# Performance work log

Measured on AMD Instinct MI355X. Metric: run time of the kernel, lower is better.

## Reference

```python
import jax, jax.numpy as jnp
import numpy as np

HIDDEN = 32          # hardcoded in nn.Linear(latent_dim, 32)
THRESHOLD = 1.5      # hardcoded adjacency threshold


def setup_inputs() -> dict:
    key = jax.random.key(0)
    ks = jax.random.split(key, 12)
    N, LATENT, MSG = 8192, 128, 64

    def lin(kw, kb, fan_in, fan_out):
        bound = 1.0 / np.sqrt(fan_in)
        W = jax.random.uniform(kw, (fan_in, fan_out), jnp.float32, -bound, bound)
        b = jax.random.uniform(kb, (fan_out,), jnp.float32, -bound, bound)
        return W, b

    enc_W, enc_b = lin(ks[0], ks[1], LATENT, HIDDEN)
    msg_W, msg_b = lin(ks[2], ks[3], HIDDEN, MSG)
    upd_W, upd_b = lin(ks[4], ks[5], HIDDEN + MSG, HIDDEN)
    out_W, out_b = lin(ks[6], ks[7], HIDDEN, MSG)

    z = jax.random.normal(ks[8], (N, LATENT), jnp.float32)
    agent_dists = jax.random.normal(ks[9], (N, N), jnp.float32)
    tau = jnp.float32(1.0)
    return {
        "z": z, "tau": tau, "agent_dists": agent_dists,
        "enc_W": enc_W, "enc_b": enc_b,
        "msg_W": msg_W, "msg_b": msg_b,
        "upd_W": upd_W, "upd_b": upd_b,
        "out_W": out_W, "out_b": out_b,
    }


def reference(z, tau, agent_dists, enc_W, enc_b, msg_W, msg_b, upd_W, upd_b, out_W, out_b):
    N = agent_dists.shape[0]
    h = jax.nn.relu(z @ enc_W + enc_b)                       # [N, 32]
    # vectorized adjacency: off-diagonal entries with dist < threshold
    idx = jnp.arange(N)
    off_diag = idx[:, None] != idx[None, :]
    adj = jnp.where(off_diag & (agent_dists < THRESHOLD), 1.0, 0.0).astype(z.dtype)  # [N, N]
    messages = h @ msg_W + msg_b                             # [N, MSG]
    aggregated = adj @ messages                              # [N, MSG]
    h2 = jax.nn.relu(jnp.concatenate([h, aggregated], axis=-1) @ upd_W + upd_b)  # [N, 32]
    logits = h2 @ out_W + out_b                              # [N, MSG]
    # gumbel_softmax (soft): softmax((logits + gumbel) / tau)
    gkey = jax.random.key(42)
    u = jax.random.uniform(gkey, logits.shape, logits.dtype, 1e-10, 1.0)
    gumbel = -jnp.log(-jnp.log(u))
    return jax.nn.softmax((logits + gumbel) / tau, axis=-1)
```

## Files before the change

### kernel.cpp

```cpp
#include <hip/hip_runtime.h>
#include <hip/hip_bf16.h>
#include <math.h>

#define N_AGENTS 8192
#define LATENT   128
#define HIDDEN   32
#define MSG      64
#define CONCAT   96
#define THRESH   1.5f
#define NPART    16
#define ROWSTRIDE 260

typedef float f32x4  __attribute__((ext_vector_type(4)));
typedef short bf16x8 __attribute__((ext_vector_type(8)));

__device__ __forceinline__ unsigned rotl32(unsigned x, unsigned r) {
  return (x << r) | (x >> (32u - r));
}
__device__ __forceinline__ void tf_round(unsigned &x0, unsigned &x1, unsigned r) {
  x0 += x1; x1 = rotl32(x1, r); x1 ^= x0;
}
__device__ __forceinline__ uint2 threefry_0_42(unsigned x0, unsigned x1) {
  const unsigned k0 = 0u, k1 = 42u, k2 = 0x1BD11BDAu ^ 0u ^ 42u;
  x0 += k0; x1 += k1;
  tf_round(x0,x1,13); tf_round(x0,x1,15); tf_round(x0,x1,26); tf_round(x0,x1, 6);
  x0 += k1; x1 += k2 + 1u;
  tf_round(x0,x1,17); tf_round(x0,x1,29); tf_round(x0,x1,16); tf_round(x0,x1,24);
  x0 += k2; x1 += k0 + 2u;
  tf_round(x0,x1,13); tf_round(x0,x1,15); tf_round(x0,x1,26); tf_round(x0,x1, 6);
  x0 += k0; x1 += k1 + 3u;
  tf_round(x0,x1,17); tf_round(x0,x1,29); tf_round(x0,x1,16); tf_round(x0,x1,24);
  x0 += k1; x1 += k2 + 4u;
  tf_round(x0,x1,13); tf_round(x0,x1,15); tf_round(x0,x1,26); tf_round(x0,x1, 6);
  x0 += k2; x1 += k0 + 5u;
  return make_uint2(x0, x1);
}

__device__ __forceinline__ float gumbel_at(unsigned idx) {
  const unsigned H = (N_AGENTS * MSG) / 2;
  unsigned bits;
  if (idx < H) {
    uint2 o = threefry_0_42(idx, idx + H);
    bits = o.x;
  } else {
    uint2 o = threefry_0_42(idx - H, idx);
    bits = o.y;
  }
  float f = __uint_as_float((bits >> 9) | 0x3f800000u) - 1.0f;
  float u = fmaxf(1e-10f, f + 1e-10f);
  return -logf(-logf(u));
}

__device__ __forceinline__ unsigned short f2bf(float x) {
  unsigned u = __float_as_uint(x);
  u += 0x7FFFu + ((u >> 16) & 1u);
  return (unsigned short)(u >> 16);
}

__device__ __forceinline__ void stage16(const float* g, float* l) {
  __builtin_amdgcn_global_load_lds(
      (const __attribute__((address_space(1))) void*)g,
      (__attribute__((address_space(3))) void*)l, 16, 0, 0);
}

__global__ __launch_bounds__(256) void k_encode(
    const float* __restrict__ z, const float* __restrict__ encW, const float* __restrict__ encB,
    const float* __restrict__ msgW, const float* __restrict__ msgB,
    float* __restrict__ h_out, unsigned* __restrict__ msgR_u32,
    unsigned short* __restrict__ msgT)
{
  __shared__ float z_s[8][LATENT];
  __shared__ float encW_s[LATENT*HIDDEN];
  __shared__ float msgW_s[HIDDEN*MSG];
  __shared__ float h_s[8][HIDDEN];
  __shared__ float m_s[8][MSG];
  const int t  = threadIdx.x;
  const int r0 = blockIdx.x * 8;

  #pragma unroll
  for (int it = 0; it < 16; ++it) encW_s[t + 256*it] = encW[t + 256*it];
  #pragma unroll
  for (int it = 0; it < 8; ++it)  msgW_s[t + 256*it] = msgW[t + 256*it];
  #pragma unroll
  for (int it = 0; it < 4; ++it) {
    int q = t + 256*it;
    z_s[q >> 7][q & 127] = z[(size_t)r0*LATENT + q];
  }
  __syncthreads();

  {
    int r = t >> 5, c = t & 31;
    float acc = encB[c];
    #pragma unroll
    for (int k = 0; k < LATENT; ++k) acc = fmaf(z_s[r][k], encW_s[k*HIDDEN + c], acc);
    float hv = fmaxf(acc, 0.0f);
    h_s[r][c] = hv;
    h_out[(size_t)(r0 + r)*HIDDEN + c] = hv;
  }
  __syncthreads();

  #pragma unroll
  for (int it = 0; it < 2; ++it) {
    int r = (t >> 6) + 4*it, c = t & 63;
    float acc = msgB[c];
    #pragma unroll
    for (int k = 0; k < HIDDEN; ++k) acc = fmaf(h_s[r][k], msgW_s[k*MSG + c], acc);
    m_s[r][c] = acc;
  }
  __syncthreads();

  {
    int r = t >> 5, c0 = (t & 31) * 2;
    unsigned lo = f2bf(m_s[r][c0]), hi = f2bf(m_s[r][c0 + 1]);
    msgR_u32[(size_t)(r0 + r)*32 + (t & 31)] = lo | (hi << 16);
  }
  {
    int c = t & 63, rr = (t >> 6) * 2;
    unsigned lo = f2bf(m_s[rr][c]), hi = f2bf(m_s[rr + 1][c]);
    *(unsigned*)(msgT + (size_t)c*N_AGENTS + r0 + rr) = lo | (hi << 16);
  }
}

__device__ __forceinline__ bf16x8 adj_frag(f32x4 lo, f32x4 hi) {
  union { bf16x8 v; unsigned u[4]; } r;
  r.u[0] = (lo.x < THRESH ? 0x3F80u : 0u) | (lo.y < THRESH ? 0x3F800000u : 0u);
  r.u[1] = (lo.z < THRESH ? 0x3F80u : 0u) | (lo.w < THRESH ? 0x3F800000u : 0u);
  r.u[2] = (hi.x < THRESH ? 0x3F80u : 0u) | (hi.y < THRESH ? 0x3F800000u : 0u);
  r.u[3] = (hi.z < THRESH ? 0x3F80u : 0u) | (hi.w < THRESH ? 0x3F800000u : 0u);
  return r.v;
}

__global__ __launch_bounds__(256, 4) void k_agg(
    const float* __restrict__ dists, const unsigned short* __restrict__ msgT,
    float* __restrict__ P)
{
  __shared__ __align__(16) float ldsA[32 * ROWSTRIDE];
  const int lane = threadIdx.x & 63;
  const int wv   = threadIdx.x >> 6;
  const int rowTile  = blockIdx.x & 255;
  const int sliceGrp = blockIdx.x >> 8;
  const int row0 = rowTile * 32;
  const int kblk = sliceGrp * 2048;
  const int m = lane & 15, q = lane >> 4;

  f32x4 acc[2][4];
  #pragma unroll
  for (int g = 0; g < 2; ++g)
    #pragma unroll
    for (int nt = 0; nt < 4; ++nt) acc[g][nt] = (f32x4)0.0f;

  const unsigned short* bbase = msgT + (size_t)m * N_AGENTS;

  for (int chunk = 0; chunk < 8; ++chunk) {
    const int kb = kblk + chunk * 256;
    #pragma unroll
    for (int rr = 0; rr < 8; ++rr) {
      const int r = wv * 8 + rr;
      stage16(dists + (size_t)(row0 + r) * N_AGENTS + kb + lane * 4,
              &ldsA[r * ROWSTRIDE]);
    }
    __syncthreads();

    #pragma unroll
    for (int ks = 0; ks < 2; ++ks) {
      const int kf = wv * 64 + ks * 32 + q * 8;
      f32x4 a00 = *(const f32x4*)&ldsA[m * ROWSTRIDE + kf];
      f32x4 a01 = *(const f32x4*)&ldsA[m * ROWSTRIDE + kf + 4];
      f32x4 a10 = *(const f32x4*)&ldsA[(m + 16) * ROWSTRIDE + kf];
      f32x4 a11 = *(const f32x4*)&ldsA[(m + 16) * ROWSTRIDE + kf + 4];
      bf16x8 af0 = adj_frag(a00, a01);
      bf16x8 af1 = adj_frag(a10, a11);
      const size_t kg = (size_t)kb + kf;
      bf16x8 b0 = *(const bf16x8*)(bbase + (size_t)0  * N_AGENTS + kg);
      bf16x8 b1 = *(const bf16x8*)(bbase + (size_t)16 * N_AGENTS + kg);
      bf16x8 b2 = *(const bf16x8*)(bbase + (size_t)32 * N_AGENTS + kg);
      bf16x8 b3 = *(const bf16x8*)(bbase + (size_t)48 * N_AGENTS + kg);
      acc[0][0] = __builtin_amdgcn_mfma_f32_16x16x32_bf16(af0, b0, acc[0][0], 0, 0, 0);
      acc[0][1] = __builtin_amdgcn_mfma_f32_16x16x32_bf16(af0, b1, acc[0][1], 0, 0, 0);
      acc[0][2] = __builtin_amdgcn_mfma_f32_16x16x32_bf16(af0, b2, acc[0][2], 0, 0, 0);
      acc[0][3] = __builtin_amdgcn_mfma_f32_16x16x32_bf16(af0, b3, acc[0][3], 0, 0, 0);
      acc[1][0] = __builtin_amdgcn_mfma_f32_16x16x32_bf16(af1, b0, acc[1][0], 0, 0, 0);
      acc[1][1] = __builtin_amdgcn_mfma_f32_16x16x32_bf16(af1, b1, acc[1][1], 0, 0, 0);
      acc[1][2] = __builtin_amdgcn_mfma_f32_16x16x32_bf16(af1, b2, acc[1][2], 0, 0, 0);
      acc[1][3] = __builtin_amdgcn_mfma_f32_16x16x32_bf16(af1, b3, acc[1][3], 0, 0, 0);
    }
    __syncthreads();
  }

  float* dst = P + (size_t)(sliceGrp * 4 + wv) * N_AGENTS * MSG;
  #pragma unroll
  for (int g = 0; g < 2; ++g)
    #pragma unroll
    for (int nt = 0; nt < 4; ++nt)
      #pragma unroll
      for (int r = 0; r < 4; ++r)
        dst[(size_t)(row0 + g*16 + q*4 + r) * MSG + nt*16 + m] = acc[g][nt][r];
}

__global__ __launch_bounds__(256) void k_out(
    const float* __restrict__ P, const float* __restrict__ dists,
    const unsigned short* __restrict__ msgR,
    const float* __restrict__ h_in,
    const float* __restrict__ updW, const float* __restrict__ updB,
    const float* __restrict__ outW, const float* __restrict__ outB,
    const float* __restrict__ tau, float* __restrict__ out)
{
  __shared__ float x_s[4][CONCAT];
  __shared__ float h2_s[4][HIDDEN];
  const int w    = threadIdx.x >> 6;
  const int lane = threadIdx.x & 63;
  const int i    = blockIdx.x * 4 + w;

  float agg = 0.0f;
  #pragma unroll
  for (int g = 0; g < NPART; ++g)
    agg += P[((size_t)g * N_AGENTS + i) * MSG + lane];

  float dii = dists[(size_t)i * (N_AGENTS + 1)];
  if (dii < THRESH) {
    unsigned short us = msgR[(size_t)i * MSG + lane];
    agg -= __uint_as_float(((unsigned)us) << 16);
  }

  x_s[w][HIDDEN + lane] = agg;
  if (lane < HIDDEN) x_s[w][lane] = h_in[(size_t)i * HIDDEN + lane];
  __syncthreads();

  if (lane < HIDDEN) {
    float acc = updB[lane];
    #pragma unroll
    for (int k = 0; k < CONCAT; ++k) acc = fmaf(x_s[w][k], updW[k*HIDDEN + lane], acc);
    h2_s[w][lane] = fmaxf(acc, 0.0f);
  }
  __syncthreads();

  float lg = outB[lane];
  #pragma unroll
  for (int c = 0; c < HIDDEN; ++c) lg = fmaf(h2_s[w][c], outW[c*MSG + lane], lg);

  float tv = (lg + gumbel_at((unsigned)i*64u + (unsigned)lane)) / tau[0];

  float mx = tv;
  #pragma unroll
  for (int off = 32; off > 0; off >>= 1) mx = fmaxf(mx, __shfl_xor(mx, off, 64));
  float ex = expf(tv - mx);
  float sm = ex;
  #pragma unroll
  for (int off = 32; off > 0; off >>= 1) sm += __shfl_xor(sm, off, 64);
  out[(size_t)i * MSG + lane] = ex / sm;
}

extern "C" void kernel_launch(void* const* d_in, const int* in_sizes, int n_in,
                              void* d_out, int out_size, void* d_ws, size_t ws_size,
                              hipStream_t stream) {
  const float* z     = (const float*)d_in[0];
  const float* tau   = (const float*)d_in[1];
  const float* dists = (const float*)d_in[2];
  const float* encW  = (const float*)d_in[3];
  const float* encB  = (const float*)d_in[4];
  const float* msgW  = (const float*)d_in[5];
  const float* msgB  = (const float*)d_in[6];
  const float* updW  = (const float*)d_in[7];
  const float* updB  = (const float*)d_in[8];
  const float* outW  = (const float*)d_in[9];
  const float* outB  = (const float*)d_in[10];
  (void)in_sizes; (void)n_in; (void)out_size; (void)ws_size;

  char* ws = (char*)d_ws;
  float*          P_ws  = (float*)(ws);
  float*          h_ws  = (float*)(ws + (32u<<20));
  unsigned short* msgR  = (unsigned short*)(ws + (33u<<20));
  unsigned short* msgT  = (unsigned short*)(ws + (34u<<20));
  float* out = (float*)d_out;

  hipLaunchKernelGGL(k_encode, dim3(N_AGENTS/8), dim3(256), 0, stream,
                     z, encW, encB, msgW, msgB, h_ws, (unsigned*)msgR, msgT);
  hipLaunchKernelGGL(k_agg, dim3(256 * 4), dim3(256), 0, stream,
                     dists, msgT, P_ws);
  hipLaunchKernelGGL(k_out, dim3(N_AGENTS/4), dim3(256), 0, stream,
                     P_ws, dists, msgR, h_ws, updW, updB, outW, outB, tau, out);
}
```

Measured before the change: 418.5 us.

## Fuse aggregation and output MLP into one kernel with double-buffered dist staging

Merges the adjacency-aggregation kernel and the output/update/softmax kernel. Each block now owns 16 full rows across the whole K dimension, so the 16-way partial-sum buffer written to global memory and re-read by a second kernel goes away, along with one launch. It also double-buffers the dists tiles in LDS so the next chunk loads while the current one is computed. The trade-off is fewer, longer-running blocks (512 instead of 1024) and a larger LDS footprint per block, which may lower occupancy and memory parallelism on the dominant 256MB dists stream.

```diff
diff --git a/kernel.cpp b/kernel.cpp
--- a/kernel.cpp
+++ b/kernel.cpp
@@ -1,5 +1,4 @@
 #include <hip/hip_runtime.h>
-#include <hip/hip_bf16.h>
 #include <math.h>
 
 #define N_AGENTS 8192
@@ -8,8 +7,11 @@
 #define MSG      64
 #define CONCAT   96
 #define THRESH   1.5f
-#define NPART    16
-#define ROWSTRIDE 260
+
+#define ROWS     16
+#define CHUNK    512
+#define NCHUNK   (N_AGENTS / CHUNK)
+#define RSTR     516
 
 typedef float f32x4  __attribute__((ext_vector_type(4)));
 typedef short bf16x8 __attribute__((ext_vector_type(8)));
@@ -130,124 +132,129 @@
   return r.v;
 }
 
-__global__ __launch_bounds__(256, 4) void k_agg(
+__global__ __launch_bounds__(256, 2) void k_fused(
     const float* __restrict__ dists, const unsigned short* __restrict__ msgT,
-    float* __restrict__ P)
+    const unsigned short* __restrict__ msgR, const float* __restrict__ h_in,
+    const float* __restrict__ updW, const float* __restrict__ updB,
+    const float* __restrict__ outW, const float* __restrict__ outB,
+    const float* __restrict__ tau, float* __restrict__ out)
 {
-  __shared__ __align__(16) float ldsA[32 * ROWSTRIDE];
+  __shared__ __align__(16) float S[2 * ROWS * RSTR];
   const int lane = threadIdx.x & 63;
   const int wv   = threadIdx.x >> 6;
-  const int rowTile  = blockIdx.x & 255;
-  const int sliceGrp = blockIdx.x >> 8;
-  const int row0 = rowTile * 32;
-  const int kblk = sliceGrp * 2048;
   const int m = lane & 15, q = lane >> 4;
-
-  f32x4 acc[2][4];
-  #pragma unroll
-  for (int g = 0; g < 2; ++g)
-    #pragma unroll
-    for (int nt = 0; nt < 4; ++nt) acc[g][nt] = (f32x4)0.0f;
+  const int row0 = blockIdx.x * ROWS;
+  const int wvK  = wv * 128;
+
+  f32x4 acc[4];
+  #pragma unroll
+  for (int nt = 0; nt < 4; ++nt) acc[nt] = (f32x4)0.0f;
 
   const unsigned short* bbase = msgT + (size_t)m * N_AGENTS;
 
-  for (int chunk = 0; chunk < 8; ++chunk) {
-    const int kb = kblk + chunk * 256;
-    #pragma unroll
-    for (int rr = 0; rr < 8; ++rr) {
-      const int r = wv * 8 + rr;
-      stage16(dists + (size_t)(row0 + r) * N_AGENTS + kb + lane * 4,
-              &ldsA[r * ROWSTRIDE]);
-    }
-    __syncthreads();
-
-    #pragma unroll
-    for (int ks = 0; ks < 2; ++ks) {
-      const int kf = wv * 64 + ks * 32 + q * 8;
-      f32x4 a00 = *(const f32x4*)&ldsA[m * ROWSTRIDE + kf];
-      f32x4 a01 = *(const f32x4*)&ldsA[m * ROWSTRIDE + kf + 4];
-      f32x4 a10 = *(const f32x4*)&ldsA[(m + 16) * ROWSTRIDE + kf];
-      f32x4 a11 = *(const f32x4*)&ldsA[(m + 16) * ROWSTRIDE + kf + 4];
-      bf16x8 af0 = adj_frag(a00, a01);
-      bf16x8 af1 = adj_frag(a10, a11);
-      const size_t kg = (size_t)kb + kf;
+  #pragma unroll
+  for (int rr = 0; rr < 4; ++rr) {
+    const int r = wv * 4 + rr;
+    const float* gsrc = dists + (size_t)(row0 + r) * N_AGENTS;
+    stage16(gsrc + lane * 4,       &S[r * RSTR]);
+    stage16(gsrc + 256 + lane * 4, &S[r * RSTR + 256]);
+  }
+  __syncthreads();
+
+  for (int c = 0; c < NCHUNK; ++c) {
+    float* buf = &S[(c & 1) * ROWS * RSTR];
+    if (c + 1 < NCHUNK) {
+      float* nbuf = &S[((c + 1) & 1) * ROWS * RSTR];
+      const int cb = (c + 1) * CHUNK;
+      #pragma unroll
+      for (int rr = 0; rr < 4; ++rr) {
+        const int r = wv * 4 + rr;
+        const float* gsrc = dists + (size_t)(row0 + r) * N_AGENTS + cb;
+        stage16(gsrc + lane * 4,       &nbuf[r * RSTR]);
+        stage16(gsrc + 256 + lane * 4, &nbuf[r * RSTR + 256]);
+      }
+    }
+    const int cb0 = c * CHUNK;
+    #pragma unroll
+    for (int ks = 0; ks < 4; ++ks) {
+      const int kf = wvK + ks * 32 + q * 8;
+      f32x4 a0 = *(const f32x4*)&buf[m * RSTR + kf];
+      f32x4 a1 = *(const f32x4*)&buf[m * RSTR + kf + 4];
+      bf16x8 af = adj_frag(a0, a1);
+      const size_t kg = (size_t)cb0 + kf;
       bf16x8 b0 = *(const bf16x8*)(bbase + (size_t)0  * N_AGENTS + kg);
       bf16x8 b1 = *(const bf16x8*)(bbase + (size_t)16 * N_AGENTS + kg);
       bf16x8 b2 = *(const bf16x8*)(bbase + (size_t)32 * N_AGENTS + kg);
       bf16x8 b3 = *(const bf16x8*)(bbase + (size_t)48 * N_AGENTS + kg);
-      acc[0][0] = __builtin_amdgcn_mfma_f32_16x16x32_bf16(af0, b0, acc[0][0], 0, 0, 0);
-      acc[0][1] = __builtin_amdgcn_mfma_f32_16x16x32_bf16(af0, b1, acc[0][1], 0, 0, 0);
-      acc[0][2] = __builtin_amdgcn_mfma_f32_16x16x32_bf16(af0, b2, acc[0][2], 0, 0, 0);
-      acc[0][3] = __builtin_amdgcn_mfma_f32_16x16x32_bf16(af0, b3, acc[0][3], 0, 0, 0);
-      acc[1][0] = __builtin_amdgcn_mfma_f32_16x16x32_bf16(af1, b0, acc[1][0], 0, 0, 0);
-      acc[1][1] = __builtin_amdgcn_mfma_f32_16x16x32_bf16(af1, b1, acc[1][1], 0, 0, 0);
-      acc[1][2] = __builtin_amdgcn_mfma_f32_16x16x32_bf16(af1, b2, acc[1][2], 0, 0, 0);
-      acc[1][3] = __builtin_amdgcn_mfma_f32_16x16x32_bf16(af1, b3, acc[1][3], 0, 0, 0);
+      acc[0] = __builtin_amdgcn_mfma_f32_16x16x32_bf16(af, b0, acc[0], 0, 0, 0);
+      acc[1] = __builtin_amdgcn_mfma_f32_16x16x32_bf16(af, b1, acc[1], 0, 0, 0);
+      acc[2] = __builtin_amdgcn_mfma_f32_16x16x32_bf16(af, b2, acc[2], 0, 0, 0);
+      acc[3] = __builtin_amdgcn_mfma_f32_16x16x32_bf16(af, b3, acc[3], 0, 0, 0);
     }
     __syncthreads();
   }
 
-  float* dst = P + (size_t)(sliceGrp * 4 + wv) * N_AGENTS * MSG;
-  #pragma unroll
-  for (int g = 0; g < 2; ++g)
-    #pragma unroll
-    for (int nt = 0; nt < 4; ++nt)
+  float* part = S;
+  #pragma unroll
+  for (int nt = 0; nt < 4; ++nt)
+    #pragma unroll
+    for (int r = 0; r < 4; ++r)
+      part[wv * 1024 + (q * 4 + r) * 64 + nt * 16 + m] = acc[nt][r];
+  __syncthreads();
+
+  float* x_s  = &S[8192];
+  float* h2_s = &S[8192 + 16 * CONCAT];
+  const float tauv = tau[0];
+
+  #pragma unroll
+  for (int rr = 0; rr < 4; ++rr) {
+    const int r16 = wv * 4 + rr;
+    const int i = row0 + r16;
+    float agg = part[0 * 1024 + r16 * 64 + lane]
+              + part[1 * 1024 + r16 * 64 + lane]
+              + part[2 * 1024 + r16 * 64 + lane]
+              + part[3 * 1024 + r16 * 64 + lane];
+    float dii = dists[(size_t)i * (N_AGENTS + 1)];
+    if (dii < THRESH) {
+      unsigned short us = msgR[(size_t)i * MSG + lane];
+      agg -= __uint_as_float(((unsigned)us) << 16);
+    }
+    x_s[r16 * CONCAT + HIDDEN + lane] = agg;
+    if (lane < HIDDEN) x_s[r16 * CONCAT + lane] = h_in[(size_t)i * HIDDEN + lane];
+  }
+
+  #pragma unroll
+  for (int rr = 0; rr < 4; ++rr) {
+    const int r16 = wv * 4 + rr;
+    if (lane < HIDDEN) {
+      float a2 = updB[lane];
       #pragma unroll
-      for (int r = 0; r < 4; ++r)
-        dst[(size_t)(row0 + g*16 + q*4 + r) * MSG + nt*16 + m] = acc[g][nt][r];
-}
-
-__global__ __launch_bounds__(256) void k_out(
-    const float* __restrict__ P, const float* __restrict__ dists,
-    const unsigned short* __restrict__ msgR,
-    const float* __restrict__ h_in,
-    const float* __restrict__ updW, const float* __restrict__ updB,
-    const float* __restrict__ outW, const float* __restrict__ outB,
-    const float* __restrict__ tau, float* __restrict__ out)
-{
-  __shared__ float x_s[4][CONCAT];
-  __shared__ float h2_s[4][HIDDEN];
-  const int w    = threadIdx.x >> 6;
-  const int lane = threadIdx.x & 63;
-  const int i    = blockIdx.x * 4 + w;
-
-  float agg = 0.0f;
-  #pragma unroll
-  for (int g = 0; g < NPART; ++g)
-    agg += P[((size_t)g * N_AGENTS + i) * MSG + lane];
-
-  float dii = dists[(size_t)i * (N_AGENTS + 1)];
-  if (dii < THRESH) {
-    unsigned short us = msgR[(size_t)i * MSG + lane];
-    agg -= __uint_as_float(((unsigned)us) << 16);
-  }
-
-  x_s[w][HIDDEN + lane] = agg;
-  if (lane < HIDDEN) x_s[w][lane] = h_in[(size_t)i * HIDDEN + lane];
-  __syncthreads();
-
-  if (lane < HIDDEN) {
-    float acc = updB[lane];
-    #pragma unroll
-    for (int k = 0; k < CONCAT; ++k) acc = fmaf(x_s[w][k], updW[k*HIDDEN + lane], acc);
-    h2_s[w][lane] = fmaxf(acc, 0.0f);
-  }
-  __syncthreads();
-
-  float lg = outB[lane];
-  #pragma unroll
-  for (int c = 0; c < HIDDEN; ++c) lg = fmaf(h2_s[w][c], outW[c*MSG + lane], lg);
-
-  float tv = (lg + gumbel_at((unsigned)i*64u + (unsigned)lane)) / tau[0];
-
-  float mx = tv;
-  #pragma unroll
-  for (int off = 32; off > 0; off >>= 1) mx = fmaxf(mx, __shfl_xor(mx, off, 64));
-  float ex = expf(tv - mx);
-  float sm = ex;
-  #pragma unroll
-  for (int off = 32; off > 0; off >>= 1) sm += __shfl_xor(sm, off, 64);
-  out[(size_t)i * MSG + lane] = ex / sm;
+      for (int k = 0; k < CONCAT; ++k)
+        a2 = fmaf(x_s[r16 * CONCAT + k], updW[k * HIDDEN + lane], a2);
+      h2_s[r16 * HIDDEN + lane] = fmaxf(a2, 0.0f);
+    }
+  }
+
+  #pragma unroll
+  for (int rr = 0; rr < 4; ++rr) {
+    const int r16 = wv * 4 + rr;
+    const int i = row0 + r16;
+    float lg = outB[lane];
+    #pragma unroll
+    for (int c = 0; c < HIDDEN; ++c)
+      lg = fmaf(h2_s[r16 * HIDDEN + c], outW[c * MSG + lane], lg);
+
+    float tv = (lg + gumbel_at((unsigned)i * 64u + (unsigned)lane)) / tauv;
+
+    float mx = tv;
+    #pragma unroll
+    for (int off = 32; off > 0; off >>= 1) mx = fmaxf(mx, __shfl_xor(mx, off, 64));
+    float ex = expf(tv - mx);
+    float sm = ex;
+    #pragma unroll
+    for (int off = 32; off > 0; off >>= 1) sm += __shfl_xor(sm, off, 64);
+    out[(size_t)i * MSG + lane] = ex / sm;
+  }
 }
 
 extern "C" void kernel_launch(void* const* d_in, const int* in_sizes, int n_in,
@@ -267,16 +274,13 @@
   (void)in_sizes; (void)n_in; (void)out_size; (void)ws_size;
 
   char* ws = (char*)d_ws;
-  float*          P_ws  = (float*)(ws);
-  float*          h_ws  = (float*)(ws + (32u<<20));
-  unsigned short* msgR  = (unsigned short*)(ws + (33u<<20));
-  unsigned short* msgT  = (unsigned short*)(ws + (34u<<20));
+  float*          h_ws  = (float*)(ws);
+  unsigned short* msgR  = (unsigned short*)(ws + (1u<<20));
+  unsigned short* msgT  = (unsigned short*)(ws + (2u<<20));
   float* out = (float*)d_out;
 
   hipLaunchKernelGGL(k_encode, dim3(N_AGENTS/8), dim3(256), 0, stream,
                      z, encW, encB, msgW, msgB, h_ws, (unsigned*)msgR, msgT);
-  hipLaunchKernelGGL(k_agg, dim3(256 * 4), dim3(256), 0, stream,
-                     dists, msgT, P_ws);
-  hipLaunchKernelGGL(k_out, dim3(N_AGENTS/4), dim3(256), 0, stream,
-                     P_ws, dists, msgR, h_ws, updW, updB, outW, outB, tau, out);
-}
+  hipLaunchKernelGGL(k_fused, dim3(N_AGENTS/ROWS), dim3(256), 0, stream,
+                     dists, msgT, msgR, h_ws, updW, updB, outW, outB, tau, out);
+}
```

After: 416.7 us. About the same (-0.4%).
